# Performance work log

Measured on AMD Instinct MI355X. Metric: run time of the kernel, lower is better.

Reference implementation:

```python
import jax, jax.numpy as jnp
import numpy as np

N_TOTAL = 2_000_000   # total particles across all events
N_EVENTS = 20_000     # number of events (segments)
H = 64                # phi/rho hidden width
OUT = 10              # output classes


def _lin(x, W, b):
    # torch nn.Linear: y = x @ W.T + b
    return x @ W.T + b


def setup_inputs() -> dict:
    key = jax.random.key(0)
    ks = jax.random.split(key, 24)
    s = 0.1  # small init scale
    inp = {
        "values": jax.random.normal(ks[0], (N_TOTAL,), dtype=jnp.float32),
        "seg_ids": jnp.sort(jax.random.randint(ks[1], (N_TOTAL,), 0, N_EVENTS)),
        "p1w0": jax.random.normal(ks[2], (H, 1), dtype=jnp.float32) * s,
        "p1b0": jax.random.normal(ks[3], (H,), dtype=jnp.float32) * s,
        "p1w1": jax.random.normal(ks[4], (H, H), dtype=jnp.float32) * s,
        "p1b1": jax.random.normal(ks[5], (H,), dtype=jnp.float32) * s,
        "r1w0": jax.random.normal(ks[6], (H, H), dtype=jnp.float32) * s,
        "r1b0": jax.random.normal(ks[7], (H,), dtype=jnp.float32) * s,
        "r1w1": jax.random.normal(ks[8], (H, H), dtype=jnp.float32) * s,
        "r1b1": jax.random.normal(ks[9], (H,), dtype=jnp.float32) * s,
        "o1w": jax.random.normal(ks[10], (H, H), dtype=jnp.float32) * s,
        "o1b": jax.random.normal(ks[11], (H,), dtype=jnp.float32) * s,
        "p2w0": jax.random.normal(ks[12], (H, H), dtype=jnp.float32) * s,
        "p2b0": jax.random.normal(ks[13], (H,), dtype=jnp.float32) * s,
        "p2w1": jax.random.normal(ks[14], (H, H), dtype=jnp.float32) * s,
        "p2b1": jax.random.normal(ks[15], (H,), dtype=jnp.float32) * s,
        "r2w0": jax.random.normal(ks[16], (H, H), dtype=jnp.float32) * s,
        "r2b0": jax.random.normal(ks[17], (H,), dtype=jnp.float32) * s,
        "r2w1": jax.random.normal(ks[18], (H, H), dtype=jnp.float32) * s,
        "r2b1": jax.random.normal(ks[19], (H,), dtype=jnp.float32) * s,
        "o2w": jax.random.normal(ks[20], (OUT, H), dtype=jnp.float32) * s,
        "o2b": jax.random.normal(ks[21], (OUT,), dtype=jnp.float32) * s,
    }
    return inp


def reference(values, seg_ids, p1w0, p1b0, p1w1, p1b1, r1w0, r1b0, r1w1, r1b1,
              o1w, o1b, p2w0, p2b0, p2w1, p2b1, r2w0, r2b0, r2w1, r2b1, o2w, o2b):
    relu = jax.nn.relu
    # stage 1: phi1 on each scalar particle value -> [N, H]
    h = relu(_lin(values[:, None], p1w0, p1b0))
    h = relu(_lin(h, p1w1, p1b1))
    # jagged sum over particles within each event (the inner deepset sum)
    ev = jax.ops.segment_sum(h, seg_ids, num_segments=N_EVENTS)  # [E, H]
    # rho1 + output linear + activation per event
    ev = relu(_lin(ev, r1w0, r1b0))
    ev = relu(_lin(ev, r1w1, r1b1))
    ev = relu(_lin(ev, o1w, o1b))  # [E, H] (output_size of deepset1 = rho_sizes[-1])
    # stage 2: phi2 per event, sum over all events
    h2 = relu(_lin(ev, p2w0, p2b0))
    h2 = relu(_lin(h2, p2w1, p2b1))
    s2 = jnp.sum(h2, axis=0, keepdims=True)  # [1, H]
    r2 = relu(_lin(s2, r2w0, r2b0))
    r2 = relu(_lin(r2, r2w1, r2b1))
    out = _lin(r2, o2w, o2b)  # [1, OUT]
    return jax.nn.log_softmax(out, axis=1)
```

## Files before the change

kernel.cpp:

```cpp
#include <hip/hip_runtime.h>

#define NT 2000000
#define NE 20000
#define NT4 (NT / 4)
#define K1_BLOCKS 1024
#define K1_WAVES (K1_BLOCKS * 4)
#define K2_BLOCKS ((NE + 63) / 64)

using bf16x8 = __attribute__((ext_vector_type(8))) __bf16;
using half8  = __attribute__((ext_vector_type(8))) _Float16;
using half2v = __attribute__((ext_vector_type(2))) _Float16;
using f32x4  = __attribute__((ext_vector_type(4))) float;
using f32x2  = __attribute__((ext_vector_type(2))) float;
using fvec4  = __attribute__((ext_vector_type(4))) float;

__device__ __forceinline__ half8 load_h8(const float* __restrict__ p) {
    fvec4 a = *(const fvec4*)p;
    fvec4 b = *(const fvec4*)(p + 4);
    half8 r;
#pragma unroll
    for (int e = 0; e < 4; e++) {
        r[e]     = (_Float16)a[e];
        r[e + 4] = (_Float16)b[e];
    }
    return r;
}

__global__ __launch_bounds__(256) void k0_offsets(
    const int* __restrict__ seg, int* __restrict__ off, float* __restrict__ s2,
    int* __restrict__ counter) {
    if (blockIdx.x == 0) {
        if (threadIdx.x < 64) s2[threadIdx.x] = 0.f;
        if (threadIdx.x == 64) *counter = 0;
    }
    const int g = blockIdx.x * 256 + threadIdx.x;
    if (g >= NT4) return;
    const int idx4 = g * 4;
    const int4 s = *(const int4*)(seg + idx4);
    int prev = (g == 0) ? -1 : seg[idx4 - 1];
    int vals[4] = {s.x, s.y, s.z, s.w};
#pragma unroll
    for (int k = 0; k < 4; k++) {
        const int cur = vals[k];
        if (cur != prev) {
            for (int e = prev + 1; e <= cur; ++e) off[e] = idx4 + k;
        }
        prev = cur;
    }
    if (idx4 + 3 == NT - 1) {
        for (int e = prev + 1; e <= NE; ++e) off[e] = NT;
    }
}

__global__ __launch_bounds__(256, 4) void k1_phi1(
    const float* __restrict__ values, const int* __restrict__ off,
    const float* __restrict__ w0, const float* __restrict__ b0,
    const float* __restrict__ w1, const float* __restrict__ b1,
    float* __restrict__ ev) {
    const int tid = threadIdx.x;
    const int w   = tid >> 6;
    const int l   = tid & 63;
    const int l15 = l & 15;
    const int l4  = l >> 4;

    half8 Bh[2][4];
#pragma unroll
    for (int kf = 0; kf < 2; kf++)
#pragma unroll
        for (int jf = 0; jf < 4; jf++)
            Bh[kf][jf] = load_h8(w1 + (jf * 16 + l15) * 64 + kf * 32 + l4 * 8);

    half2v w0h[2][4], b0h[2][4];
#pragma unroll
    for (int kf = 0; kf < 2; kf++) {
        const int kb = kf * 32 + l4 * 8;
#pragma unroll
        for (int e2 = 0; e2 < 4; e2++) {
            f32x2 wp = *(const f32x2*)(w0 + kb + 2 * e2);
            f32x2 bp = *(const f32x2*)(b0 + kb + 2 * e2);
            w0h[kf][e2] = half2v{(_Float16)wp[0], (_Float16)wp[1]};
            b0h[kf][e2] = half2v{(_Float16)bp[0], (_Float16)bp[1]};
        }
    }
    f32x4 biasC[4];
#pragma unroll
    for (int jf = 0; jf < 4; jf++) {
        const float bj = b1[jf * 16 + l15];
#pragma unroll
        for (int r = 0; r < 4; r++) biasC[jf][r] = bj;
    }

    auto buildA = [&](_Float16 v, half8& A0, half8& A1) {
        const half2v vv = {v, v};
#pragma unroll
        for (int e2 = 0; e2 < 4; e2++) {
            half2v h0 = vv * w0h[0][e2] + b0h[0][e2];
            half2v h1 = vv * w0h[1][e2] + b0h[1][e2];
            const _Float16 z = (_Float16)0.f;
            A0[2 * e2]     = h0[0] > z ? h0[0] : z;
            A0[2 * e2 + 1] = h0[1] > z ? h0[1] : z;
            A1[2 * e2]     = h1[0] > z ? h1[0] : z;
            A1[2 * e2 + 1] = h1[1] > z ? h1[1] : z;
        }
    };
    auto chain = [&](const half8& A0, const half8& A1, float* sj) {
#pragma unroll
        for (int jf = 0; jf < 4; jf++) {
            f32x4 tt = __builtin_amdgcn_mfma_f32_16x16x32_f16(
                A0, Bh[0][jf], biasC[jf], 0, 0, 0);
            tt = __builtin_amdgcn_mfma_f32_16x16x32_f16(
                A1, Bh[1][jf], tt, 0, 0, 0);
            sj[jf] += (fmaxf(tt[0], 0.f) + fmaxf(tt[1], 0.f)) +
                      (fmaxf(tt[2], 0.f) + fmaxf(tt[3], 0.f));
        }
    };
    auto chainTail = [&](const half8& A0, const half8& A1, float* sj, int rem) {
#pragma unroll
        for (int jf = 0; jf < 4; jf++) {
            f32x4 tt = __builtin_amdgcn_mfma_f32_16x16x32_f16(
                A0, Bh[0][jf], biasC[jf], 0, 0, 0);
            tt = __builtin_amdgcn_mfma_f32_16x16x32_f16(
                A1, Bh[1][jf], tt, 0, 0, 0);
            float s = 0.f;
#pragma unroll
            for (int r = 0; r < 4; r++) {
                const bool ok = (l4 * 4 + r) < rem;
                s += ok ? fmaxf(tt[r], 0.f) : 0.f;
            }
            sj[jf] += s;
        }
    };

    const bool bit0 = (l & 16) != 0;
    const bool bit1 = (l & 32) != 0;
    auto reduce4 = [&](const float sj[4]) -> float {
        float send01 = bit0 ? sj[0] : sj[1];
        float keep01 = bit0 ? sj[1] : sj[0];
        float c01 = keep01 + __shfl_xor(send01, 16);
        float send23 = bit0 ? sj[2] : sj[3];
        float keep23 = bit0 ? sj[3] : sj[2];
        float c23 = keep23 + __shfl_xor(send23, 16);
        float send = bit1 ? c01 : c23;
        float keep = bit1 ? c23 : c01;
        return keep + __shfl_xor(send, 32);
    };

    const int wid = blockIdx.x * 4 + w;

    for (int e = wid; e < NE; e += K1_WAVES) {
        const int s = off[e];
        const int t = off[e + 1];
        const int n = t - s;
        const int nfull = n >> 4;
        const float* vp = values + s + l15;

        float sjA[4] = {0.f, 0.f, 0.f, 0.f};
        float sjB[4] = {0.f, 0.f, 0.f, 0.f};

        int b = 0;
        for (; b + 2 <= nfull; b += 2) {
            const _Float16 vA = (_Float16)vp[b * 16];
            const _Float16 vB = (_Float16)vp[b * 16 + 16];
            half8 A0A, A1A, A0B, A1B;
            buildA(vA, A0A, A1A);
            buildA(vB, A0B, A1B);
            chain(A0A, A1A, sjA);
            chain(A0B, A1B, sjB);
        }
        if (b < nfull) {
            const _Float16 vA = (_Float16)vp[b * 16];
            half8 A0A, A1A;
            buildA(vA, A0A, A1A);
            chain(A0A, A1A, sjA);
        }
        const int rem = n & 15;
        if (rem) {
            const _Float16 vA =
                (_Float16)((l15 < rem) ? vp[nfull * 16] : 0.f);
            half8 A0A, A1A;
            buildA(vA, A0A, A1A);
            chainTail(A0A, A1A, sjA, rem);
        }

        float sj[4];
#pragma unroll
        for (int jf = 0; jf < 4; jf++) sj[jf] = sjA[jf] + sjB[jf];
        ev[(size_t)e * 64 + l] = reduce4(sj);
    }
}

__global__ __launch_bounds__(64) void k2_events(
    const float* __restrict__ ev,
    const float* __restrict__ W0, const float* __restrict__ B0,
    const float* __restrict__ W1, const float* __restrict__ B1,
    const float* __restrict__ W2, const float* __restrict__ B2,
    const float* __restrict__ W3, const float* __restrict__ B3,
    const float* __restrict__ W4, const float* __restrict__ B4,
    float* __restrict__ s2, int* __restrict__ counter,
    const float* __restrict__ R0, const float* __restrict__ Rb0,
    const float* __restrict__ R1, const float* __restrict__ Rb1,
    const float* __restrict__ OW, const float* __restrict__ OB,
    float* __restrict__ out) {
    __shared__ __align__(16) _Float16 xt[64 * 72];
    const int l   = threadIdx.x;
    const int l15 = l & 15;
    const int l4  = l >> 4;
    const int ebase = blockIdx.x * 64;

    const float* Ws[5] = {W0, W1, W2, W3, W4};
    const float* Bs[5] = {B0, B1, B2, B3, B4};

    half8 A[4][2];
#pragma unroll
    for (int pf = 0; pf < 4; pf++) {
        const int e = ebase + pf * 16 + l15;
#pragma unroll
        for (int kf = 0; kf < 2; kf++) {
            half8 a;
            if (e < NE) {
                a = load_h8(ev + (size_t)e * 64 + kf * 32 + l4 * 8);
            } else {
#pragma unroll
                for (int e2 = 0; e2 < 8; e2++) a[e2] = (_Float16)0.f;
            }
            A[pf][kf] = a;
        }
    }

#pragma unroll
    for (int L = 0; L < 5; L++) {
        half8 Bh[2][4];
#pragma unroll
        for (int kf = 0; kf < 2; kf++)
#pragma unroll
            for (int jf = 0; jf < 4; jf++)
                Bh[kf][jf] = load_h8(Ws[L] + (jf * 16 + l15) * 64 +
                                     kf * 32 + l4 * 8);

        f32x4 acc[4][4];
#pragma unroll
        for (int jf = 0; jf < 4; jf++) {
            const float bj = Bs[L][jf * 16 + l15];
#pragma unroll
            for (int pf = 0; pf < 4; pf++)
#pragma unroll
                for (int r = 0; r < 4; r++) acc[pf][jf][r] = bj;
        }
#pragma unroll
        for (int kf = 0; kf < 2; kf++)
#pragma unroll
            for (int pf = 0; pf < 4; pf++)
#pragma unroll
                for (int jf = 0; jf < 4; jf++)
                    acc[pf][jf] = __builtin_amdgcn_mfma_f32_16x16x32_f16(
                        A[pf][kf], Bh[kf][jf], acc[pf][jf], 0, 0, 0);

        if (L < 4) {
#pragma unroll
            for (int pf = 0; pf < 4; pf++)
#pragma unroll
                for (int jf = 0; jf < 4; jf++) {
                    const int j = jf * 16 + l15;
#pragma unroll
                    for (int r = 0; r < 4; r++)
                        xt[(pf * 16 + l4 * 4 + r) * 72 + j] =
                            (_Float16)fmaxf(acc[pf][jf][r], 0.f);
                }
#pragma unroll
            for (int pf = 0; pf < 4; pf++)
#pragma unroll
                for (int kf = 0; kf < 2; kf++)
                    A[pf][kf] = *(const half8*)(xt + (pf * 16 + l15) * 72 +
                                                kf * 32 + l4 * 8);
        } else {
            float sj[4];
#pragma unroll
            for (int jf = 0; jf < 4; jf++) {
                float s = 0.f;
#pragma unroll
                for (int pf = 0; pf < 4; pf++)
#pragma unroll
                    for (int r = 0; r < 4; r++) {
                        const int e = ebase + pf * 16 + l4 * 4 + r;
                        float v = fmaxf(acc[pf][jf][r], 0.f);
                        s += (e < NE) ? v : 0.f;
                    }
                s += __shfl_xor(s, 16);
                s += __shfl_xor(s, 32);
                sj[jf] = s;
            }
            float v = (l4 == 0) ? sj[0] : (l4 == 1) ? sj[1]
                    : (l4 == 2) ? sj[2] : sj[3];
            atomicAdd(s2 + l, v);
        }
    }

    __shared__ int is_last;
    __threadfence();
    if (l == 0) {
        const int c = atomicAdd(counter, 1);
        is_last = (c == (int)gridDim.x - 1);
    }
    __syncthreads();
    if (!is_last) return;

    __shared__ __align__(16) float xb[64];
    __shared__ __align__(16) float yb[64];
    __shared__ float ob[10];

    xb[l] = atomicAdd(s2 + l, 0.f);
    __syncthreads();

    float a0 = Rb0[l];
#pragma unroll
    for (int k = 0; k < 16; k++) {
        fvec4 wv = *(const fvec4*)(R0 + l * 64 + k * 4);
        fvec4 xv = *(const fvec4*)(xb + k * 4);
        a0 += wv[0] * xv[0] + wv[1] * xv[1] + wv[2] * xv[2] + wv[3] * xv[3];
    }
    yb[l] = fmaxf(a0, 0.f);
    __syncthreads();

    float b_ = Rb1[l];
#pragma unroll
    for (int k = 0; k < 16; k++) {
        fvec4 wv = *(const fvec4*)(R1 + l * 64 + k * 4);
        fvec4 xv = *(const fvec4*)(yb + k * 4);
        b_ += wv[0] * xv[0] + wv[1] * xv[1] + wv[2] * xv[2] + wv[3] * xv[3];
    }
    __syncthreads();
    xb[l] = fmaxf(b_, 0.f);
    __syncthreads();

    if (l < 10) {
        float o = OB[l];
#pragma unroll
        for (int k = 0; k < 16; k++) {
            fvec4 wv = *(const fvec4*)(OW + l * 64 + k * 4);
            fvec4 xv = *(const fvec4*)(xb + k * 4);
            o += wv[0] * xv[0] + wv[1] * xv[1] + wv[2] * xv[2] + wv[3] * xv[3];
        }
        ob[l] = o;
    }
    __syncthreads();
    if (l == 0) {
        float m = ob[0];
#pragma unroll
        for (int i = 1; i < 10; i++) m = fmaxf(m, ob[i]);
        float sum = 0.f;
#pragma unroll
        for (int i = 0; i < 10; i++) sum = sum + expf(ob[i] - m);
        float ls = logf(sum);
#pragma unroll
        for (int i = 0; i < 10; i++) out[i] = ob[i] - m - ls;
    }
}

extern "C" void kernel_launch(void* const* d_in, const int* in_sizes, int n_in,
                              void* d_out, int out_size, void* d_ws, size_t ws_size,
                              hipStream_t stream) {
    const float* values = (const float*)d_in[0];
    const int*   seg    = (const int*)d_in[1];
    const float* p1w0 = (const float*)d_in[2],  *p1b0 = (const float*)d_in[3];
    const float* p1w1 = (const float*)d_in[4],  *p1b1 = (const float*)d_in[5];
    const float* r1w0 = (const float*)d_in[6],  *r1b0 = (const float*)d_in[7];
    const float* r1w1 = (const float*)d_in[8],  *r1b1 = (const float*)d_in[9];
    const float* o1w  = (const float*)d_in[10], *o1b  = (const float*)d_in[11];
    const float* p2w0 = (const float*)d_in[12], *p2b0 = (const float*)d_in[13];
    const float* p2w1 = (const float*)d_in[14], *p2b1 = (const float*)d_in[15];
    const float* r2w0 = (const float*)d_in[16], *r2b0 = (const float*)d_in[17];
    const float* r2w1 = (const float*)d_in[18], *r2b1 = (const float*)d_in[19];
    const float* o2w  = (const float*)d_in[20], *o2b  = (const float*)d_in[21];

    float* ev  = (float*)d_ws;
    float* s2  = ev + (size_t)NE * 64;
    int*   off = (int*)(s2 + 64);
    int*   counter = off + (NE + 1);

    hipLaunchKernelGGL(k0_offsets, dim3((NT4 + 255) / 256), dim3(256), 0, stream,
                       seg, off, s2, counter);
    hipLaunchKernelGGL(k1_phi1, dim3(K1_BLOCKS), dim3(256), 0, stream,
                       values, off, p1w0, p1b0, p1w1, p1b1, ev);
    hipLaunchKernelGGL(k2_events, dim3(K2_BLOCKS), dim3(64), 0, stream,
                       ev, r1w0, r1b0, r1w1, r1b1, o1w, o1b,
                       p2w0, p2b0, p2w1, p2b1, s2, counter,
                       r2w0, r2b0, r2w1, r2b1, o2w, o2b, (float*)d_out);
}
```

Baseline: 67.94 us.

## Replace phi1 MFMA chain with piecewise-linear lookup tables over input breakpoints

Because phi1's first layer takes a scalar input, it is piecewise linear. A new precompute kernel sorts the 64 ReLU breakpoints and builds, for each of the 65 intervals, the folded second-layer slope and intercept per output unit. The phi1 kernel then finds each value's interval with a ballot/popcount against the sorted breakpoints and evaluates one fma plus ReLU per lane, instead of two layers of f16 MFMAs. This removes the matmul work and the f16 precision loss, but processes particles serially per wave (one shuffle, ballot and LDS lookup each). It also adds an extra kernel launch and staging of a 33 KB table in shared memory.

```diff
diff --git a/kernel.cpp b/kernel.cpp
--- a/kernel.cpp
+++ b/kernel.cpp
@@ -6,12 +6,10 @@
 #define K1_BLOCKS 1024
 #define K1_WAVES (K1_BLOCKS * 4)
 #define K2_BLOCKS ((NE + 63) / 64)
-
-using bf16x8 = __attribute__((ext_vector_type(8))) __bf16;
+#define NSEG 65
+
 using half8  = __attribute__((ext_vector_type(8))) _Float16;
-using half2v = __attribute__((ext_vector_type(2))) _Float16;
 using f32x4  = __attribute__((ext_vector_type(4))) float;
-using f32x2  = __attribute__((ext_vector_type(2))) float;
 using fvec4  = __attribute__((ext_vector_type(4))) float;
 
 __device__ __forceinline__ half8 load_h8(const float* __restrict__ p) {
@@ -24,6 +22,41 @@
         r[e + 4] = (_Float16)b[e];
     }
     return r;
+}
+
+__global__ __launch_bounds__(64) void k_pre(
+    const float* __restrict__ w0, const float* __restrict__ b0,
+    const float* __restrict__ w1, const float* __restrict__ b1,
+    float* __restrict__ sorted_t, float2* __restrict__ tab) {
+    __shared__ float tS[64], w0S[64], b0S[64];
+    __shared__ int rankS[64], styleS[64];
+    const int k = threadIdx.x;
+    const float w = w0[k], b = b0[k];
+    float t; int style;
+    if (w != 0.f) { t = -b / w; style = (w > 0.f) ? 1 : 0; }
+    else          { t = (b > 0.f) ? -INFINITY : INFINITY; style = 1; }
+    tS[k] = t; w0S[k] = w; b0S[k] = b; styleS[k] = style;
+    __syncthreads();
+    int rank = 0;
+    for (int i = 0; i < 64; i++) {
+        const float ti = tS[i];
+        rank += (ti < t || (ti == t && i < k)) ? 1 : 0;
+    }
+    rankS[k] = rank;
+    __syncthreads();
+    if (blockIdx.x == 0) sorted_t[rank] = t;
+
+    const int s = blockIdx.x;
+    float a = 0.f, c = b1[k];
+    for (int kk = 0; kk < 64; kk++) {
+        const bool act = styleS[kk] ? (s > rankS[kk]) : (s <= rankS[kk]);
+        if (act) {
+            const float wjk = w1[k * 64 + kk];
+            a = fmaf(wjk, w0S[kk], a);
+            c = fmaf(wjk, b0S[kk], c);
+        }
+    }
+    tab[s * 64 + k] = make_float2(a, c);
 }
 
 __global__ __launch_bounds__(256) void k0_offsets(
@@ -52,140 +85,43 @@
     }
 }
 
-__global__ __launch_bounds__(256, 4) void k1_phi1(
+__global__ __launch_bounds__(256) void k1_phi1(
     const float* __restrict__ values, const int* __restrict__ off,
-    const float* __restrict__ w0, const float* __restrict__ b0,
-    const float* __restrict__ w1, const float* __restrict__ b1,
+    const float* __restrict__ sorted_t, const float2* __restrict__ gtab,
     float* __restrict__ ev) {
+    __shared__ __align__(16) float2 tab[NSEG * 64];
     const int tid = threadIdx.x;
-    const int w   = tid >> 6;
-    const int l   = tid & 63;
-    const int l15 = l & 15;
-    const int l4  = l >> 4;
-
-    half8 Bh[2][4];
-#pragma unroll
-    for (int kf = 0; kf < 2; kf++)
-#pragma unroll
-        for (int jf = 0; jf < 4; jf++)
-            Bh[kf][jf] = load_h8(w1 + (jf * 16 + l15) * 64 + kf * 32 + l4 * 8);
-
-    half2v w0h[2][4], b0h[2][4];
-#pragma unroll
-    for (int kf = 0; kf < 2; kf++) {
-        const int kb = kf * 32 + l4 * 8;
-#pragma unroll
-        for (int e2 = 0; e2 < 4; e2++) {
-            f32x2 wp = *(const f32x2*)(w0 + kb + 2 * e2);
-            f32x2 bp = *(const f32x2*)(b0 + kb + 2 * e2);
-            w0h[kf][e2] = half2v{(_Float16)wp[0], (_Float16)wp[1]};
-            b0h[kf][e2] = half2v{(_Float16)bp[0], (_Float16)bp[1]};
-        }
-    }
-    f32x4 biasC[4];
-#pragma unroll
-    for (int jf = 0; jf < 4; jf++) {
-        const float bj = b1[jf * 16 + l15];
-#pragma unroll
-        for (int r = 0; r < 4; r++) biasC[jf][r] = bj;
-    }
-
-    auto buildA = [&](_Float16 v, half8& A0, half8& A1) {
-        const half2v vv = {v, v};
-#pragma unroll
-        for (int e2 = 0; e2 < 4; e2++) {
-            half2v h0 = vv * w0h[0][e2] + b0h[0][e2];
-            half2v h1 = vv * w0h[1][e2] + b0h[1][e2];
-            const _Float16 z = (_Float16)0.f;
-            A0[2 * e2]     = h0[0] > z ? h0[0] : z;
-            A0[2 * e2 + 1] = h0[1] > z ? h0[1] : z;
-            A1[2 * e2]     = h1[0] > z ? h1[0] : z;
-            A1[2 * e2 + 1] = h1[1] > z ? h1[1] : z;
-        }
-    };
-    auto chain = [&](const half8& A0, const half8& A1, float* sj) {
-#pragma unroll
-        for (int jf = 0; jf < 4; jf++) {
-            f32x4 tt = __builtin_amdgcn_mfma_f32_16x16x32_f16(
-                A0, Bh[0][jf], biasC[jf], 0, 0, 0);
-            tt = __builtin_amdgcn_mfma_f32_16x16x32_f16(
-                A1, Bh[1][jf], tt, 0, 0, 0);
-            sj[jf] += (fmaxf(tt[0], 0.f) + fmaxf(tt[1], 0.f)) +
-                      (fmaxf(tt[2], 0.f) + fmaxf(tt[3], 0.f));
-        }
-    };
-    auto chainTail = [&](const half8& A0, const half8& A1, float* sj, int rem) {
-#pragma unroll
-        for (int jf = 0; jf < 4; jf++) {
-            f32x4 tt = __builtin_amdgcn_mfma_f32_16x16x32_f16(
-                A0, Bh[0][jf], biasC[jf], 0, 0, 0);
-            tt = __builtin_amdgcn_mfma_f32_16x16x32_f16(
-                A1, Bh[1][jf], tt, 0, 0, 0);
-            float s = 0.f;
-#pragma unroll
-            for (int r = 0; r < 4; r++) {
-                const bool ok = (l4 * 4 + r) < rem;
-                s += ok ? fmaxf(tt[r], 0.f) : 0.f;
+    const int w = tid >> 6, l = tid & 63;
+
+    for (int idx = tid; idx < NSEG * 64; idx += 256) tab[idx] = gtab[idx];
+    const float t_l = sorted_t[l];
+    __syncthreads();
+
+    const int wid = blockIdx.x * 4 + w;
+    for (int e = wid; e < NE; e += K1_WAVES) {
+        const int ps = off[e], pe = off[e + 1];
+        float sjA = 0.f, sjB = 0.f;
+        for (int base = ps; base < pe; base += 64) {
+            const int cnt = pe - base;
+            const float v_l = (base + l < pe) ? values[base + l] : 0.f;
+#pragma unroll
+            for (int i = 0; i < 64; i += 2) {
+                if (i >= cnt) break;
+                {
+                    const float vs = __shfl(v_l, i);
+                    const int sg = (int)__popcll(__ballot(vs > t_l));
+                    const float2 ac = tab[sg * 64 + l];
+                    sjA += fmaxf(fmaf(ac.x, vs, ac.y), 0.f);
+                }
+                if (i + 1 < cnt) {
+                    const float vs = __shfl(v_l, i + 1);
+                    const int sg = (int)__popcll(__ballot(vs > t_l));
+                    const float2 ac = tab[sg * 64 + l];
+                    sjB += fmaxf(fmaf(ac.x, vs, ac.y), 0.f);
+                }
             }
-            sj[jf] += s;
-        }
-    };
-
-    const bool bit0 = (l & 16) != 0;
-    const bool bit1 = (l & 32) != 0;
-    auto reduce4 = [&](const float sj[4]) -> float {
-        float send01 = bit0 ? sj[0] : sj[1];
-        float keep01 = bit0 ? sj[1] : sj[0];
-        float c01 = keep01 + __shfl_xor(send01, 16);
-        float send23 = bit0 ? sj[2] : sj[3];
-        float keep23 = bit0 ? sj[3] : sj[2];
-        float c23 = keep23 + __shfl_xor(send23, 16);
-        float send = bit1 ? c01 : c23;
-        float keep = bit1 ? c23 : c01;
-        return keep + __shfl_xor(send, 32);
-    };
-
-    const int wid = blockIdx.x * 4 + w;
-
-    for (int e = wid; e < NE; e += K1_WAVES) {
-        const int s = off[e];
-        const int t = off[e + 1];
-        const int n = t - s;
-        const int nfull = n >> 4;
-        const float* vp = values + s + l15;
-
-        float sjA[4] = {0.f, 0.f, 0.f, 0.f};
-        float sjB[4] = {0.f, 0.f, 0.f, 0.f};
-
-        int b = 0;
-        for (; b + 2 <= nfull; b += 2) {
-            const _Float16 vA = (_Float16)vp[b * 16];
-            const _Float16 vB = (_Float16)vp[b * 16 + 16];
-            half8 A0A, A1A, A0B, A1B;
-            buildA(vA, A0A, A1A);
-            buildA(vB, A0B, A1B);
-            chain(A0A, A1A, sjA);
-            chain(A0B, A1B, sjB);
-        }
-        if (b < nfull) {
-            const _Float16 vA = (_Float16)vp[b * 16];
-            half8 A0A, A1A;
-            buildA(vA, A0A, A1A);
-            chain(A0A, A1A, sjA);
-        }
-        const int rem = n & 15;
-        if (rem) {
-            const _Float16 vA =
-                (_Float16)((l15 < rem) ? vp[nfull * 16] : 0.f);
-            half8 A0A, A1A;
-            buildA(vA, A0A, A1A);
-            chainTail(A0A, A1A, sjA, rem);
-        }
-
-        float sj[4];
-#pragma unroll
-        for (int jf = 0; jf < 4; jf++) sj[jf] = sjA[jf] + sjB[jf];
-        ev[(size_t)e * 64 + l] = reduce4(sj);
+        }
+        ev[(size_t)e * 64 + l] = sjA + sjB;
     }
 }
 
@@ -372,15 +308,19 @@
     const float* r2w1 = (const float*)d_in[18], *r2b1 = (const float*)d_in[19];
     const float* o2w  = (const float*)d_in[20], *o2b  = (const float*)d_in[21];
 
-    float* ev  = (float*)d_ws;
-    float* s2  = ev + (size_t)NE * 64;
-    int*   off = (int*)(s2 + 64);
-    int*   counter = off + (NE + 1);
-
+    float*  ev       = (float*)d_ws;
+    float*  s2       = ev + (size_t)NE * 64;
+    int*    off      = (int*)(s2 + 64);
+    int*    counter  = off + (NE + 1);
+    float*  sorted_t = (float*)(counter + 1);
+    float2* tab      = (float2*)(sorted_t + 64);
+
+    hipLaunchKernelGGL(k_pre, dim3(NSEG), dim3(64), 0, stream,
+                       p1w0, p1b0, p1w1, p1b1, sorted_t, tab);
     hipLaunchKernelGGL(k0_offsets, dim3((NT4 + 255) / 256), dim3(256), 0, stream,
                        seg, off, s2, counter);
     hipLaunchKernelGGL(k1_phi1, dim3(K1_BLOCKS), dim3(256), 0, stream,
-                       values, off, p1w0, p1b0, p1w1, p1b1, ev);
+                       values, off, sorted_t, tab, ev);
     hipLaunchKernelGGL(k2_events, dim3(K2_BLOCKS), dim3(64), 0, stream,
                        ev, r1w0, r1b0, r1w1, r1b1, o1w, o1b,
                        p2w0, p2b0, p2w1, p2b1, s2, counter,
```

New measurement: 99.06 us. 45.8% more time.
